# Optimization experiments

Hardware: AMD Instinct MI355X
Metric: run time of the kernel (lower is better)

Reference implementation:

```python
import jax, jax.numpy as jnp
import numpy as np

DIM = 1024
STATE = 64
HEADS = 8
EXPAND = 2
INNER = DIM * EXPAND          # 2048
HEAD_DIM = INNER // HEADS     # 256
KERNEL = 4
B, L = 2, 2048
EPS = 1e-5


def setup_inputs() -> dict:
    key = jax.random.key(0)
    ks = jax.random.split(key, 12)
    s = 0.02
    return {
        "input_tensor": jax.random.normal(ks[0], (B, L, DIM), jnp.float32),
        "Wx": jax.random.normal(ks[1], (INNER, DIM), jnp.float32) * s,
        "Wz": jax.random.normal(ks[2], (INNER, DIM), jnp.float32) * s,
        "conv_w": jax.random.normal(ks[3], (INNER, 1, KERNEL), jnp.float32) * s,
        "conv_b": jnp.zeros((INNER,), jnp.float32),
        "Wb": jax.random.normal(ks[4], (HEADS * STATE, INNER), jnp.float32) * s,
        "Wc": jax.random.normal(ks[5], (HEADS * STATE, INNER), jnp.float32) * s,
        "Wdt": jax.random.normal(ks[6], (HEADS, INNER), jnp.float32) * s,
        "b_dt": jnp.zeros((HEADS,), jnp.float32),
        "log_a": jnp.log(jnp.full((HEADS,), 0.5, jnp.float32)),
        "d_param": jnp.ones((HEADS,), jnp.float32),
        "gn_w": jnp.ones((INNER,), jnp.float32),
        "gn_b": jnp.zeros((INNER,), jnp.float32),
        "Wout": jax.random.normal(ks[7], (DIM, INNER), jnp.float32) * s,
    }


def _causal_conv(x, conv_w, conv_b):
    # x: (B, L, INNER); depthwise conv, kernel 4, left-pad 3 (causal)
    x_pad = jnp.pad(x, ((0, 0), (KERNEL - 1, 0), (0, 0)))
    w = conv_w[:, 0, :]  # (INNER, K)
    y = sum(x_pad[:, k:k + x.shape[1], :] * w[:, k] for k in range(KERNEL))
    return y + conv_b


def _ssd_scan(x, b, c, dt, a):
    # x: (B,L,H,P) b,c: (B,L,H,N) dt: (B,L,H) a: (H,)
    state0 = jnp.zeros((x.shape[0], HEADS, STATE, HEAD_DIM), x.dtype)

    def step(state, inp):
        x_t, b_t, c_t, dt_t = inp  # (B,H,P),(B,H,N),(B,H,N),(B,H)
        decay = jnp.exp(dt_t * a)[..., None, None]          # (B,H,1,1)
        b_bar = (dt_t[..., None] * b_t)                      # (B,H,N)
        state = decay * state + b_bar[..., None] * x_t[:, :, None, :]
        y_t = jnp.einsum("bhn,bhnp->bhp", c_t, state)
        return state, y_t

    xs = (x.transpose(1, 0, 2, 3), b.transpose(1, 0, 2, 3),
          c.transpose(1, 0, 2, 3), dt.transpose(1, 0, 2))
    _, ys = jax.lax.scan(step, state0, xs)  # ys: (L,B,H,P)
    return ys.transpose(1, 0, 2, 3)


def reference(input_tensor, Wx, Wz, conv_w, conv_b, Wb, Wc, Wdt, b_dt,
              log_a, d_param, gn_w, gn_b, Wout):
    bsz, seq, _ = input_tensor.shape
    x = input_tensor @ Wx.T               # (B,L,INNER)
    z = input_tensor @ Wz.T
    x = _causal_conv(x, conv_w, conv_b)
    x = jax.nn.silu(x)
    b = (x @ Wb.T).reshape(bsz, seq, HEADS, STATE)
    c = (x @ Wc.T).reshape(bsz, seq, HEADS, STATE)
    dt = jax.nn.softplus(x @ Wdt.T + b_dt)  # (B,L,H)
    xh = x.reshape(bsz, seq, HEADS, HEAD_DIM)
    a = -jnp.exp(log_a)
    y = _ssd_scan(xh, b, c, dt, a)
    y = y + d_param[None, None, :, None] * xh
    # GroupNorm(HEADS, INNER) applied on (B, C, L): normalize per (batch, group)
    # over (channels-in-group, sequence)
    yg = y  # (B, L, H, P) -- groups are contiguous channel blocks = heads
    mean = yg.mean(axis=(1, 3), keepdims=True)
    var = yg.var(axis=(1, 3), keepdims=True)
    yn = (yg - mean) / jnp.sqrt(var + EPS)
    yn = yn * gn_w.reshape(1, 1, HEADS, HEAD_DIM) + gn_b.reshape(1, 1, HEADS, HEAD_DIM)
    yn = yn.reshape(bsz, seq, INNER)
    out = yn * jax.nn.silu(z)
    return out @ Wout.T
```

## Files before the change

kernel.cpp:

```cpp
#include <hip/hip_runtime.h>
#include <math.h>

#define DIM_   1024
#define STATE_ 64
#define HEADS_ 8
#define INNER_ 2048
#define HDIM_  256
#define B_     2
#define L_     2048
#define M_     (B_*L_)
#define EPS_   1e-5f
#define Q_     64
#define NC_    (L_/Q_)
#define NCHUNK_ (B_*HEADS_*NC_)
#define BCS_   1024
#define XZS_   4096

typedef _Float16 f16;
typedef __attribute__((ext_vector_type(8))) _Float16 half8;
typedef __attribute__((ext_vector_type(4))) _Float16 half4;
typedef __attribute__((ext_vector_type(4))) float    f32x4;

__device__ __forceinline__ float siluf(float x) { return x / (1.f + expf(-x)); }

__device__ __forceinline__ void gload_lds16(const void* g, void* l) {
    __builtin_amdgcn_global_load_lds((const __attribute__((address_space(1))) void*)g,
                                     (__attribute__((address_space(3))) void*)l, 16, 0, 0);
}

__global__ __launch_bounds__(256) void cast_all(const float* __restrict__ in0,
                                                const float* __restrict__ Wx,
                                                const float* __restrict__ Wz,
                                                const float* __restrict__ Wb,
                                                const float* __restrict__ Wc,
                                                const float* __restrict__ Wout,
                                                f16* __restrict__ input_h,
                                                f16* __restrict__ wxz_h,
                                                f16* __restrict__ wbc_h,
                                                f16* __restrict__ wout_h) {
    int i = blockIdx.x * 256 + threadIdx.x;
    const float* src; f16* dst; int off;
    if      (i < 1048576) { src = in0;  dst = input_h;            off = i; }
    else if (i < 1572864) { src = Wx;   dst = wxz_h;              off = i - 1048576; }
    else if (i < 2097152) { src = Wz;   dst = wxz_h + 2097152;    off = i - 1572864; }
    else if (i < 2359296) { src = Wb;   dst = wbc_h;              off = i - 2097152; }
    else if (i < 2621440) { src = Wc;   dst = wbc_h + 1048576;    off = i - 2359296; }
    else                  { src = Wout; dst = wout_h;             off = i - 2621440; }
    float4 v = *(const float4*)&src[(size_t)off * 4];
    half4 o;
    o[0] = (f16)v.x; o[1] = (f16)v.y; o[2] = (f16)v.z; o[3] = (f16)v.w;
    *(half4*)&dst[(size_t)off * 4] = o;
}

template<int BN, bool OUTF16, bool SILUZ>
__global__ __launch_bounds__(256) void hgemm(const f16* __restrict__ A,
                                             const f16* __restrict__ W,
                                             void* __restrict__ Cout,
                                             int K, int N) {
    constexpr int N_FR = BN / 32;
    constexpr int NITER = (128 + BN) / 64;
    __shared__ f16 sA[128 * 32];
    __shared__ f16 sW[BN * 32];
    const int tid  = threadIdx.x;
    const int wid  = tid >> 6;
    const int lane = tid & 63;

    const int nwg = gridDim.x * gridDim.y;
    const int id0 = blockIdx.y * gridDim.x + blockIdx.x;
    const int cpx = nwg >> 3;
    const int id  = (id0 & 7) * cpx + (id0 >> 3);
    const int gxsh = __ffs(gridDim.x) - 1;
    const int bm = (id >> gxsh) * 128;
    const int bn = (id & (gridDim.x - 1)) * BN;

    const int wr = wid >> 1, wc = wid & 1;
    const int r  = lane & 15, kg = lane >> 4;

    const f16* gsrc[NITER];
    f16* ldst[NITER];
#pragma unroll
    for (int i = 0; i < NITER; ++i) {
        int slot = tid + i * 256;
        if (slot < 512) {
            int row = slot >> 2;
            int kgv = ((slot & 3) ^ ((row >> 1) & 3)) * 8;
            gsrc[i] = A + (size_t)(bm + row) * K + kgv;
        } else {
            int row = (slot - 512) >> 2;
            int kgv = ((slot & 3) ^ ((row >> 1) & 3)) * 8;
            gsrc[i] = W + (size_t)(bn + row) * K + kgv;
        }
        int slot0 = (tid & ~63) + i * 256;
        ldst[i] = (slot0 < 512) ? &sA[slot0 * 8] : &sW[(slot0 - 512) * 8];
    }

    int aoff[4], boff[N_FR];
#pragma unroll
    for (int m = 0; m < 4; ++m) {
        int arow = wr * 64 + m * 16 + r;
        aoff[m] = arow * 32 + ((kg ^ ((arow >> 1) & 3)) << 3);
    }
#pragma unroll
    for (int n = 0; n < N_FR; ++n) {
        int wrow = wc * (BN / 2) + n * 16 + r;
        boff[n] = wrow * 32 + ((kg ^ ((wrow >> 1) & 3)) << 3);
    }

    f32x4 acc[4][N_FR];
#pragma unroll
    for (int m = 0; m < 4; ++m)
#pragma unroll
        for (int n = 0; n < N_FR; ++n) acc[m][n] = (f32x4)0.f;

    for (int k0 = 0; k0 < K; k0 += 32) {
#pragma unroll
        for (int i = 0; i < NITER; ++i) gload_lds16(gsrc[i] + k0, ldst[i]);
        __syncthreads();
        half8 av[4], bv[N_FR];
#pragma unroll
        for (int m = 0; m < 4; ++m) av[m] = *(const half8*)&sA[aoff[m]];
#pragma unroll
        for (int n = 0; n < N_FR; ++n) bv[n] = *(const half8*)&sW[boff[n]];
#pragma unroll
        for (int m = 0; m < 4; ++m)
#pragma unroll
            for (int n = 0; n < N_FR; ++n)
                acc[m][n] = __builtin_amdgcn_mfma_f32_16x16x32_f16(av[m], bv[n], acc[m][n], 0, 0, 0);
        __syncthreads();
    }

#pragma unroll
    for (int m = 0; m < 4; ++m)
#pragma unroll
        for (int n = 0; n < N_FR; ++n) {
            int row0o = bm + wr * 64 + m * 16 + kg * 4;
            int col   = bn + wc * (BN / 2) + n * 16 + r;
#pragma unroll
            for (int j = 0; j < 4; ++j) {
                float v = acc[m][n][j];
                if (SILUZ && col >= INNER_) v = siluf(v);
                if (OUTF16) ((f16*)Cout)[(size_t)(row0o + j) * N + col] = (f16)v;
                else        ((float*)Cout)[(size_t)(row0o + j) * N + col] = v;
            }
        }
}

__global__ __launch_bounds__(256) void conv_silu_dt(const f16* __restrict__ xz,
                                                    const float* __restrict__ cw,
                                                    const float* __restrict__ cb,
                                                    const float* __restrict__ Wdt,
                                                    const float* __restrict__ bdt,
                                                    f16* __restrict__ xc,
                                                    float* __restrict__ dtb) {
    __shared__ float sred[4][HEADS_];
    const int m = blockIdx.x;
    const int tid = threadIdx.x;
    const int c8 = tid * 8;
    const int t = m & (L_ - 1);
    float acc[8];
    float4 wv[8];
#pragma unroll
    for (int j = 0; j < 8; ++j) { acc[j] = cb[c8 + j]; wv[j] = *(const float4*)&cw[(c8 + j) * 4]; }
#pragma unroll
    for (int k = 0; k < 4; ++k) {
        int tt = t - 3 + k;
        if (tt >= 0) {
            half8 xv = *(const half8*)&xz[(size_t)(m - 3 + k) * XZS_ + c8];
#pragma unroll
            for (int j = 0; j < 8; ++j) acc[j] += (float)xv[j] * ((const float*)&wv[j])[k];
        }
    }
    float xf[8];
    half8 o;
#pragma unroll
    for (int j = 0; j < 8; ++j) { xf[j] = siluf(acc[j]); o[j] = (f16)xf[j]; }
    *(half8*)&xc[(size_t)m * INNER_ + c8] = o;

    float p[HEADS_];
#pragma unroll
    for (int h = 0; h < HEADS_; ++h) {
        float4 w0 = *(const float4*)&Wdt[h * INNER_ + c8];
        float4 w1 = *(const float4*)&Wdt[h * INNER_ + c8 + 4];
        p[h] = xf[0]*w0.x + xf[1]*w0.y + xf[2]*w0.z + xf[3]*w0.w
             + xf[4]*w1.x + xf[5]*w1.y + xf[6]*w1.z + xf[7]*w1.w;
    }
#pragma unroll
    for (int h = 0; h < HEADS_; ++h)
#pragma unroll
        for (int off = 32; off > 0; off >>= 1)
            p[h] += __shfl_down(p[h], off, 64);
    if ((tid & 63) == 0) {
#pragma unroll
        for (int h = 0; h < HEADS_; ++h) sred[tid >> 6][h] = p[h];
    }
    __syncthreads();
    if (tid < 32) {
        float v = sred[tid >> 3][tid & 7];
        v += __shfl_down(v, 16, 32);
        v += __shfl_down(v, 8, 32);
        if (tid < 8) {
            float s = v + bdt[tid];
            dtb[(size_t)m * HEADS_ + tid] = (s > 20.f) ? s : log1pf(expf(s));
        }
    }
}

__global__ __launch_bounds__(256) void xpose_k(const f16* __restrict__ xc,
                                               f16* __restrict__ xT,
                                               float* __restrict__ gstat) {
    __shared__ f16 sT[64][72];
    const int blk = blockIdx.x;
    const int bh = blk >> 7;
    const int rem = blk & 127;
    const int tt = rem >> 2;
    const int pt = rem & 3;
    const int b = bh >> 3, h = bh & 7;
    const int tid = threadIdx.x;
    if (blk == 0 && tid < 2 * B_ * HEADS_) gstat[tid] = 0.f;
#pragma unroll
    for (int it = 0; it < 2; ++it) {
        int q = tid + it * 256;
        int tr = q >> 3;
        int p0 = (q & 7) * 8;
        half8 v = *(const half8*)&xc[(size_t)(b * L_ + tt * 64 + tr) * INNER_ + h * HDIM_ + pt * 64 + p0];
        *(half8*)&sT[tr][p0] = v;
    }
    __syncthreads();
#pragma unroll
    for (int it = 0; it < 2; ++it) {
        int q = tid + it * 256;
        int pr = q >> 3;
        int t0 = (q & 7) * 8;
        half8 v;
#pragma unroll
        for (int j = 0; j < 8; ++j) v[j] = sT[t0 + j][pr];
        *(half8*)&xT[((size_t)bh * HDIM_ + pt * 64 + pr) * L_ + tt * 64 + t0] = v;
    }
}

__global__ __launch_bounds__(256) void ssd12(const f16* __restrict__ bc,
                                             const float* __restrict__ dtb,
                                             const float* __restrict__ log_a,
                                             const f16* __restrict__ xT,
                                             f16* __restrict__ pbuf,
                                             f16* __restrict__ sloc,
                                             float* __restrict__ eAbuf,
                                             float* __restrict__ cdecay) {
    __shared__ float sA[Q_], sDt[Q_], sw[Q_];
    __shared__ f16 sB[Q_ * Q_];
    const int tid = threadIdx.x;
    const int chunk = blockIdx.x;
    const int bh = chunk / NC_;
    const int ck = chunk - bh * NC_;
    const int b = bh >> 3, h = bh & 7;
    const int m0 = b * L_ + ck * Q_;

    const int s0 = tid >> 3,        n00 = (tid & 7) * 8;
    const int s1 = (tid + 256) >> 3, n01 = (tid & 7) * 8;
    half8 bv0 = *(const half8*)&bc[(size_t)(m0 + s0) * BCS_ + h * STATE_ + n00];
    half8 bv1 = *(const half8*)&bc[(size_t)(m0 + s1) * BCS_ + h * STATE_ + n01];

    if (tid < 64) {
        float dt = dtb[(size_t)(m0 + tid) * HEADS_ + h];
        float a = -expf(log_a[h]);
        float x = dt * a;
#pragma unroll
        for (int off = 1; off < 64; off <<= 1) {
            float v = __shfl_up(x, off, 64);
            if (tid >= off) x += v;
        }
        float Alast = __shfl(x, 63, 64);
        sA[tid] = x;
        sDt[tid] = dt;
        sw[tid] = expf(Alast - x) * dt;
        eAbuf[(size_t)(m0 + tid) * HEADS_ + h] = expf(x);
        if (tid == 0) cdecay[chunk] = expf(Alast);
    }
    __syncthreads();

    {
        float w0 = sw[s0], w1 = sw[s1];
        half8 o0, o1;
#pragma unroll
        for (int j = 0; j < 8; ++j) { o0[j] = (f16)((float)bv0[j] * w0); o1[j] = (f16)((float)bv1[j] * w1); }
        *(half8*)&sB[s0 * Q_ + (n00 ^ ((s0 & 7) << 3))] = o0;
        *(half8*)&sB[s1 * Q_ + (n01 ^ ((s1 & 7) << 3))] = o1;
    }

    const int w = tid >> 6, lane = tid & 63;
    const int r = lane & 15, kg = lane >> 4;

    {
        const int ft = w;
        const f16* Crow = bc + (size_t)(m0 + ft * 16 + r) * BCS_ + 512 + h * STATE_;
        half8 a0 = *(const half8*)(Crow + kg * 8);
        half8 a1 = *(const half8*)(Crow + 32 + kg * 8);
#pragma unroll
        for (int fs = 0; fs < 4; ++fs) {
            const f16* Brow = bc + (size_t)(m0 + fs * 16 + r) * BCS_ + h * STATE_;
            half8 b0 = *(const half8*)(Brow + kg * 8);
            half8 b1 = *(const half8*)(Brow + 32 + kg * 8);
            f32x4 g = (f32x4)0.f;
            g = __builtin_amdgcn_mfma_f32_16x16x32_f16(a0, b0, g, 0, 0, 0);
            g = __builtin_amdgcn_mfma_f32_16x16x32_f16(a1, b1, g, 0, 0, 0);
            int s = fs * 16 + r;
            float As = sA[s], dts = sDt[s];
#pragma unroll
            for (int j = 0; j < 4; ++j) {
                int t = ft * 16 + kg * 4 + j;
                float val = (t >= s) ? g[j] * expf(sA[t] - As) * dts : 0.f;
                pbuf[((size_t)chunk * Q_ + t) * Q_ + s] = (f16)val;
            }
        }
    }
    __syncthreads();

    f32x4 acc[4][4];
#pragma unroll
    for (int i = 0; i < 4; ++i)
#pragma unroll
        for (int j = 0; j < 4; ++j) acc[i][j] = (f32x4)0.f;

#pragma unroll
    for (int kk = 0; kk < 2; ++kk) {
        half8 a[4], bfr[4];
#pragma unroll
        for (int pf = 0; pf < 4; ++pf) {
            int p = w * 64 + pf * 16 + r;
            a[pf] = *(const half8*)&xT[((size_t)bh * HDIM_ + p) * L_ + ck * Q_ + kk * 32 + kg * 8];
        }
#pragma unroll
        for (int nf = 0; nf < 4; ++nf) {
            int n = nf * 16 + r;
            half8 v;
#pragma unroll
            for (int j = 0; j < 8; ++j) {
                int s = kk * 32 + kg * 8 + j;
                v[j] = sB[s * Q_ + (n ^ (j << 3))];
            }
            bfr[nf] = v;
        }
#pragma unroll
        for (int pf = 0; pf < 4; ++pf)
#pragma unroll
            for (int nf = 0; nf < 4; ++nf)
                acc[pf][nf] = __builtin_amdgcn_mfma_f32_16x16x32_f16(a[pf], bfr[nf], acc[pf][nf], 0, 0, 0);
    }
#pragma unroll
    for (int pf = 0; pf < 4; ++pf)
#pragma unroll
        for (int nf = 0; nf < 4; ++nf) {
            int n = nf * 16 + r;
#pragma unroll
            for (int j = 0; j < 4; ++j) {
                int p = w * 64 + pf * 16 + kg * 4 + j;
                sloc[((size_t)chunk * HDIM_ + p) * STATE_ + n] = (f16)acc[pf][nf][j];
            }
        }
}

__global__ __launch_bounds__(256) void chunk_scan_k(f16* __restrict__ sloc,
                                                    const float* __restrict__ cdecay) {
    int bh = blockIdx.x >> 4;
    int el4 = (((blockIdx.x & 15) * 256 + threadIdx.x) << 2);
    float s0 = 0.f, s1 = 0.f, s2 = 0.f, s3 = 0.f;
    for (int c = 0; c < NC_; ++c) {
        size_t chunk = (size_t)bh * NC_ + c;
        f16* ptr = sloc + chunk * (size_t)(STATE_ * HDIM_) + el4;
        half4 v = *(const half4*)ptr;
        half4 o; o[0] = (f16)s0; o[1] = (f16)s1; o[2] = (f16)s2; o[3] = (f16)s3;
        *(half4*)ptr = o;
        float d = cdecay[chunk];
        s0 = d * s0 + (float)v[0];
        s1 = d * s1 + (float)v[1];
        s2 = d * s2 + (float)v[2];
        s3 = d * s3 + (float)v[3];
    }
}

__global__ __launch_bounds__(256) void ssd_phase3(const f16* __restrict__ bc,
                                                  const f16* __restrict__ pbuf,
                                                  const f16* __restrict__ xT,
                                                  const f16* __restrict__ sloc,
                                                  const f16* __restrict__ xch,
                                                  const float* __restrict__ eAbuf,
                                                  const float* __restrict__ dparam,
                                                  f16* __restrict__ ybuf,
                                                  float* __restrict__ gstats) {
    __shared__ float red[512];
    const int tid = threadIdx.x;
    const int chunk = blockIdx.x;
    const int bh = chunk / NC_;
    const int ck = chunk - bh * NC_;
    const int b = bh >> 3, h = bh & 7;
    const int m0 = b * L_ + ck * Q_;
    const int w = tid >> 6, lane = tid & 63;
    const int r = lane & 15, kg = lane >> 4;

    float eA[4];
#pragma unroll
    for (int ft = 0; ft < 4; ++ft)
        eA[ft] = eAbuf[(size_t)(m0 + ft * 16 + r) * HEADS_ + h];

    f32x4 acc[4][4];
#pragma unroll
    for (int i = 0; i < 4; ++i)
#pragma unroll
        for (int j = 0; j < 4; ++j) acc[i][j] = (f32x4)0.f;

#pragma unroll
    for (int ks = 0; ks < 4; ++ks) {
        half8 a[4], bfr[4];
#pragma unroll
        for (int ft = 0; ft < 4; ++ft) {
            int t = ft * 16 + r;
            if (ks < 2) {
                a[ft] = *(const half8*)&pbuf[((size_t)chunk * Q_ + t) * Q_ + ks * 32 + kg * 8];
            } else {
                half8 c = *(const half8*)&bc[(size_t)(m0 + t) * BCS_ + 512 + h * STATE_ + (ks - 2) * 32 + kg * 8];
                half8 sc;
#pragma unroll
                for (int j = 0; j < 8; ++j) sc[j] = (f16)(eA[ft] * (float)c[j]);
                a[ft] = sc;
            }
        }
#pragma unroll
        for (int pf = 0; pf < 4; ++pf) {
            int p = w * 64 + pf * 16 + r;
            if (ks < 2)
                bfr[pf] = *(const half8*)&xT[((size_t)bh * HDIM_ + p) * L_ + ck * Q_ + ks * 32 + kg * 8];
            else
                bfr[pf] = *(const half8*)&sloc[((size_t)chunk * HDIM_ + p) * STATE_ + (ks - 2) * 32 + kg * 8];
        }
#pragma unroll
        for (int ft = 0; ft < 4; ++ft)
#pragma unroll
            for (int pf = 0; pf < 4; ++pf)
                acc[ft][pf] = __builtin_amdgcn_mfma_f32_16x16x32_f16(a[ft], bfr[pf], acc[ft][pf], 0, 0, 0);
    }

    const float d = dparam[h];
    float lsum = 0.f, lsq = 0.f;
#pragma unroll
    for (int ft = 0; ft < 4; ++ft)
#pragma unroll
        for (int pf = 0; pf < 4; ++pf) {
            int p = w * 64 + pf * 16 + r;
#pragma unroll
            for (int j = 0; j < 4; ++j) {
                int t = ft * 16 + kg * 4 + j;
                size_t off = (size_t)(m0 + t) * INNER_ + h * HDIM_ + p;
                float y = acc[ft][pf][j] + d * (float)xch[off];
                ybuf[off] = (f16)y;
                lsum += y; lsq += y * y;
            }
        }
    __syncthreads();
    red[tid] = lsum; red[256 + tid] = lsq;
    __syncthreads();
    for (int st = 128; st > 0; st >>= 1) {
        if (tid < st) { red[tid] += red[tid + st]; red[256 + tid] += red[256 + tid + st]; }
        __syncthreads();
    }
    if (tid == 0) {
        atomicAdd(&gstats[bh * 2 + 0], red[0]);
        atomicAdd(&gstats[bh * 2 + 1], red[256]);
    }
}

__global__ __launch_bounds__(256) void gn_gate_h(const f16* __restrict__ ybuf,
                                                 const f16* __restrict__ xz,
                                                 const float* __restrict__ gstats,
                                                 const float* __restrict__ gnw,
                                                 const float* __restrict__ gnb,
                                                 f16* __restrict__ g) {
    int idx = blockIdx.x * 256 + threadIdx.x;
    int c8 = (idx & (INNER_/8 - 1)) * 8;
    int m = idx >> 8;
    int bh = (m >> 11) * HEADS_ + (c8 >> 8);
    const float cnt = (float)(L_ * HDIM_);
    float mean = gstats[bh*2] / cnt;
    float var  = gstats[bh*2+1] / cnt - mean*mean;
    float rstd = rsqrtf(var + EPS_);
    size_t off = (size_t)m * INNER_ + c8;
    half8 yv = *(const half8*)&ybuf[off];
    half8 zv = *(const half8*)&xz[(size_t)m * XZS_ + INNER_ + c8];
    float4 w0 = *(const float4*)&gnw[c8], w1 = *(const float4*)&gnw[c8+4];
    float4 b0 = *(const float4*)&gnb[c8], b1 = *(const float4*)&gnb[c8+4];
    float wv[8] = {w0.x, w0.y, w0.z, w0.w, w1.x, w1.y, w1.z, w1.w};
    float bv[8] = {b0.x, b0.y, b0.z, b0.w, b1.x, b1.y, b1.z, b1.w};
    half8 o;
#pragma unroll
    for (int j = 0; j < 8; ++j) {
        float v = ((float)yv[j] - mean) * rstd * wv[j] + bv[j];
        o[j] = (f16)(v * (float)zv[j]);
    }
    *(half8*)&g[off] = o;
}

extern "C" void kernel_launch(void* const* d_in, const int* in_sizes, int n_in,
                              void* d_out, int out_size, void* d_ws, size_t ws_size,
                              hipStream_t stream) {
    const float* input  = (const float*)d_in[0];
    const float* Wx     = (const float*)d_in[1];
    const float* Wz     = (const float*)d_in[2];
    const float* conv_w = (const float*)d_in[3];
    const float* conv_b = (const float*)d_in[4];
    const float* Wb     = (const float*)d_in[5];
    const float* Wc     = (const float*)d_in[6];
    const float* Wdt    = (const float*)d_in[7];
    const float* b_dt   = (const float*)d_in[8];
    const float* log_a  = (const float*)d_in[9];
    const float* d_par  = (const float*)d_in[10];
    const float* gn_w   = (const float*)d_in[11];
    const float* gn_b   = (const float*)d_in[12];
    const float* Wout   = (const float*)d_in[13];
    float* out = (float*)d_out;

    float* ws = (float*)d_ws;
    size_t off = 0;
    auto alloc = [&](size_t nfloats) { float* p = ws + off; off += (nfloats + 63) & ~(size_t)63; return p; };
    f16* input_h = (f16*)alloc((size_t)M_*DIM_/2);
    f16* wxz_h   = (f16*)alloc((size_t)XZS_*DIM_/2);
    f16* wbc_h   = (f16*)alloc((size_t)BCS_*INNER_/2);
    f16* wout_h  = (f16*)alloc((size_t)DIM_*INNER_/2);
    f16* xz_h    = (f16*)alloc((size_t)M_*XZS_/2);
    f16* xconv_h = (f16*)alloc((size_t)M_*INNER_/2);
    f16* xT_h    = (f16*)alloc((size_t)M_*INNER_/2);
    f16* gbuf_h  = (f16*)alloc((size_t)M_*INNER_/2);
    f16* bcmat_h = (f16*)alloc((size_t)M_*BCS_/2);
    f16* pbuf_h  = (f16*)alloc((size_t)NCHUNK_*Q_*Q_/2);
    f16* sloc_h  = (f16*)alloc((size_t)NCHUNK_*STATE_*HDIM_/2);
    f16* ybuf_h  = (f16*)alloc((size_t)M_*INNER_/2);
    float* dtb   = alloc((size_t)M_*HEADS_);
    float* eAb   = alloc((size_t)M_*HEADS_);
    float* cdec  = alloc((size_t)NCHUNK_);
    float* gstat = alloc((size_t)2*B_*HEADS_);

    dim3 blk(256);

    cast_all<<<12288, blk, 0, stream>>>(input, Wx, Wz, Wb, Wc, Wout,
                                        input_h, wxz_h, wbc_h, wout_h);
    hgemm<128,true,true><<<dim3(XZS_/128, M_/128), blk, 0, stream>>>(input_h, wxz_h, xz_h, DIM_, XZS_);
    conv_silu_dt<<<M_, blk, 0, stream>>>(xz_h, conv_w, conv_b, Wdt, b_dt, xconv_h, dtb);
    hgemm<64,true,false><<<dim3(BCS_/64, M_/128), blk, 0, stream>>>(xconv_h, wbc_h, bcmat_h, INNER_, BCS_);
    xpose_k<<<2048, blk, 0, stream>>>(xconv_h, xT_h, gstat);
    ssd12<<<NCHUNK_, blk, 0, stream>>>(bcmat_h, dtb, log_a, xT_h, pbuf_h, sloc_h, eAb, cdec);
    chunk_scan_k<<<256, blk, 0, stream>>>(sloc_h, cdec);
    ssd_phase3<<<NCHUNK_, blk, 0, stream>>>(bcmat_h, pbuf_h, xT_h, sloc_h, xconv_h,
                                            eAb, d_par, ybuf_h, gstat);
    gn_gate_h<<<(M_*(INNER_/8))/256, blk, 0, stream>>>(ybuf_h, xz_h, gstat, gn_w, gn_b, gbuf_h);
    hgemm<64,false,false><<<dim3(DIM_/64, M_/128), blk, 0, stream>>>(gbuf_h, wout_h, out, INNER_, DIM_);
}
```

Baseline: 363.2 us.

## Add 256x256 multi-stage GEMM for input projection and fold D skip into P

Replaces the first projection GEMM with a new 512-thread kernel that uses 256x256 tiles and a 4-slot LDS ring fed by direct global-to-LDS loads three stages ahead. It also drops the XCD-aware block swizzle from the generic GEMM. The D*x skip term moves into the diagonal of the intra-chunk P matrix, so phase 3 no longer re-reads the conv output. Risks include lower occupancy from 128 KB of LDS, and f16 rounding of the diagonal, now holding D plus the decay term.

```diff
diff --git a/kernel.cpp b/kernel.cpp
--- a/kernel.cpp
+++ b/kernel.cpp
@@ -52,7 +52,114 @@
     *(half4*)&dst[(size_t)off * 4] = o;
 }
 
-template<int BN, bool OUTF16, bool SILUZ>
+__global__ __launch_bounds__(512) void hgemm8p(const f16* __restrict__ A,
+                                               const f16* __restrict__ W,
+                                               f16* __restrict__ Cout,
+                                               int K, int N) {
+    __shared__ f16 lds[65536];
+    const int tid = threadIdx.x;
+    const int wid = tid >> 6, lane = tid & 63;
+    const int wm = wid >> 2, wn = wid & 3;
+    const int r = lane & 15, kg = lane >> 4;
+    const int bm = blockIdx.y * 256, bn = blockIdx.x * 256;
+
+    const int srow = tid >> 2;
+    const int scol = ((tid & 3) ^ ((srow >> 1) & 3)) * 8;
+    const f16* ga0 = A + (size_t)(bm + srow) * K + scol;
+    const f16* ga1 = A + (size_t)(bm + 128 + srow) * K + scol;
+    const f16* gw0 = W + (size_t)(bn + srow) * K + scol;
+    const f16* gw1 = W + (size_t)(bn + 128 + srow) * K + scol;
+    const int dbase = (tid & ~63) * 8;
+
+    int aoff[8], boff[4];
+#pragma unroll
+    for (int mf = 0; mf < 8; ++mf) {
+        int rr = wm * 128 + mf * 16 + r;
+        aoff[mf] = rr * 32 + ((kg ^ ((rr >> 1) & 3)) << 3);
+    }
+#pragma unroll
+    for (int nf = 0; nf < 4; ++nf) {
+        int wr = wn * 64 + nf * 16 + r;
+        boff[nf] = 8192 + wr * 32 + ((kg ^ ((wr >> 1) & 3)) << 3);
+    }
+
+    f32x4 acc[8][4];
+#pragma unroll
+    for (int mf = 0; mf < 8; ++mf)
+#pragma unroll
+        for (int nf = 0; nf < 4; ++nf) acc[mf][nf] = (f32x4)0.f;
+
+    const int KT = K >> 5;
+
+#pragma unroll
+    for (int kt = 0; kt < 3; ++kt) {
+        f16* base = &lds[(kt & 3) * 16384];
+        int ko = kt << 5;
+        gload_lds16(ga0 + ko, base + dbase);
+        gload_lds16(ga1 + ko, base + 4096 + dbase);
+        gload_lds16(gw0 + ko, base + 8192 + dbase);
+        gload_lds16(gw1 + ko, base + 12288 + dbase);
+    }
+    asm volatile("s_waitcnt vmcnt(8)" ::: "memory");
+    __builtin_amdgcn_s_barrier();
+    asm volatile("" ::: "memory");
+
+    for (int kt = 0; kt < KT; ++kt) {
+        f16* ring = &lds[(kt & 3) * 16384];
+        const bool st = (kt + 3) < KT;
+        f16* sbase = &lds[((kt + 3) & 3) * 16384];
+        const int sko = (kt + 3) << 5;
+
+        if (st) {
+            gload_lds16(ga0 + sko, sbase + dbase);
+            gload_lds16(ga1 + sko, sbase + 4096 + dbase);
+        }
+        half8 bfr[4], afr[4];
+#pragma unroll
+        for (int nf = 0; nf < 4; ++nf) bfr[nf] = *(const half8*)&ring[boff[nf]];
+#pragma unroll
+        for (int mf = 0; mf < 4; ++mf) afr[mf] = *(const half8*)&ring[aoff[mf]];
+#pragma unroll
+        for (int mf = 0; mf < 4; ++mf)
+#pragma unroll
+            for (int nf = 0; nf < 4; ++nf)
+                acc[mf][nf] = __builtin_amdgcn_mfma_f32_16x16x32_f16(afr[mf], bfr[nf], acc[mf][nf], 0, 0, 0);
+
+        if (st) {
+            gload_lds16(gw0 + sko, sbase + 8192 + dbase);
+            gload_lds16(gw1 + sko, sbase + 12288 + dbase);
+        }
+#pragma unroll
+        for (int mf = 0; mf < 4; ++mf) afr[mf] = *(const half8*)&ring[aoff[4 + mf]];
+#pragma unroll
+        for (int mf = 0; mf < 4; ++mf)
+#pragma unroll
+            for (int nf = 0; nf < 4; ++nf)
+                acc[4 + mf][nf] = __builtin_amdgcn_mfma_f32_16x16x32_f16(afr[mf], bfr[nf], acc[4 + mf][nf], 0, 0, 0);
+
+        if (kt + 1 < KT) {
+            asm volatile("s_waitcnt vmcnt(8)" ::: "memory");
+            __builtin_amdgcn_s_barrier();
+            asm volatile("" ::: "memory");
+        }
+    }
+
+#pragma unroll
+    for (int mf = 0; mf < 8; ++mf)
+#pragma unroll
+        for (int nf = 0; nf < 4; ++nf) {
+            int row = bm + wm * 128 + mf * 16 + kg * 4;
+            int col = bn + wn * 64 + nf * 16 + r;
+#pragma unroll
+            for (int j = 0; j < 4; ++j) {
+                float v = acc[mf][nf][j];
+                if (col >= INNER_) v = siluf(v);
+                Cout[(size_t)(row + j) * N + col] = (f16)v;
+            }
+        }
+}
+
+template<int BN, bool OUTF16>
 __global__ __launch_bounds__(256) void hgemm(const f16* __restrict__ A,
                                              const f16* __restrict__ W,
                                              void* __restrict__ Cout,
@@ -64,15 +171,8 @@
     const int tid  = threadIdx.x;
     const int wid  = tid >> 6;
     const int lane = tid & 63;
-
-    const int nwg = gridDim.x * gridDim.y;
-    const int id0 = blockIdx.y * gridDim.x + blockIdx.x;
-    const int cpx = nwg >> 3;
-    const int id  = (id0 & 7) * cpx + (id0 >> 3);
-    const int gxsh = __ffs(gridDim.x) - 1;
-    const int bm = (id >> gxsh) * 128;
-    const int bn = (id & (gridDim.x - 1)) * BN;
-
+    const int bm = blockIdx.y * 128;
+    const int bn = blockIdx.x * BN;
     const int wr = wid >> 1, wc = wid & 1;
     const int r  = lane & 15, kg = lane >> 4;
 
@@ -138,7 +238,6 @@
 #pragma unroll
             for (int j = 0; j < 4; ++j) {
                 float v = acc[m][n][j];
-                if (SILUZ && col >= INNER_) v = siluf(v);
                 if (OUTF16) ((f16*)Cout)[(size_t)(row0o + j) * N + col] = (f16)v;
                 else        ((float*)Cout)[(size_t)(row0o + j) * N + col] = v;
             }
@@ -241,6 +340,7 @@
 __global__ __launch_bounds__(256) void ssd12(const f16* __restrict__ bc,
                                              const float* __restrict__ dtb,
                                              const float* __restrict__ log_a,
+                                             const float* __restrict__ dparam,
                                              const f16* __restrict__ xT,
                                              f16* __restrict__ pbuf,
                                              f16* __restrict__ sloc,
@@ -291,6 +391,7 @@
     const int r = lane & 15, kg = lane >> 4;
 
     {
+        const float dpar = dparam[h];
         const int ft = w;
         const f16* Crow = bc + (size_t)(m0 + ft * 16 + r) * BCS_ + 512 + h * STATE_;
         half8 a0 = *(const half8*)(Crow + kg * 8);
@@ -309,6 +410,7 @@
             for (int j = 0; j < 4; ++j) {
                 int t = ft * 16 + kg * 4 + j;
                 float val = (t >= s) ? g[j] * expf(sA[t] - As) * dts : 0.f;
+                if (t == s) val += dpar;
                 pbuf[((size_t)chunk * Q_ + t) * Q_ + s] = (f16)val;
             }
         }
@@ -382,11 +484,10 @@
                                                   const f16* __restrict__ pbuf,
                                                   const f16* __restrict__ xT,
                                                   const f16* __restrict__ sloc,
-                                                  const f16* __restrict__ xch,
                                                   const float* __restrict__ eAbuf,
-                                                  const float* __restrict__ dparam,
-                                                  f16* __restrict__ ybuf,
+                                                  float* __restrict__ ybuf16_,
                                                   float* __restrict__ gstats) {
+    f16* ybuf = (f16*)ybuf16_;
     __shared__ float red[512];
     const int tid = threadIdx.x;
     const int chunk = blockIdx.x;
@@ -439,7 +540,6 @@
                 acc[ft][pf] = __builtin_amdgcn_mfma_f32_16x16x32_f16(a[ft], bfr[pf], acc[ft][pf], 0, 0, 0);
     }
 
-    const float d = dparam[h];
     float lsum = 0.f, lsq = 0.f;
 #pragma unroll
     for (int ft = 0; ft < 4; ++ft)
@@ -450,7 +550,7 @@
             for (int j = 0; j < 4; ++j) {
                 int t = ft * 16 + kg * 4 + j;
                 size_t off = (size_t)(m0 + t) * INNER_ + h * HDIM_ + p;
-                float y = acc[ft][pf][j] + d * (float)xch[off];
+                float y = acc[ft][pf][j];
                 ybuf[off] = (f16)y;
                 lsum += y; lsq += y * y;
             }
@@ -541,14 +641,14 @@
 
     cast_all<<<12288, blk, 0, stream>>>(input, Wx, Wz, Wb, Wc, Wout,
                                         input_h, wxz_h, wbc_h, wout_h);
-    hgemm<128,true,true><<<dim3(XZS_/128, M_/128), blk, 0, stream>>>(input_h, wxz_h, xz_h, DIM_, XZS_);
+    hgemm8p<<<dim3(XZS_/256, M_/256), dim3(512), 0, stream>>>(input_h, wxz_h, xz_h, DIM_, XZS_);
     conv_silu_dt<<<M_, blk, 0, stream>>>(xz_h, conv_w, conv_b, Wdt, b_dt, xconv_h, dtb);
-    hgemm<64,true,false><<<dim3(BCS_/64, M_/128), blk, 0, stream>>>(xconv_h, wbc_h, bcmat_h, INNER_, BCS_);
+    hgemm<64,true><<<dim3(BCS_/64, M_/128), blk, 0, stream>>>(xconv_h, wbc_h, bcmat_h, INNER_, BCS_);
     xpose_k<<<2048, blk, 0, stream>>>(xconv_h, xT_h, gstat);
-    ssd12<<<NCHUNK_, blk, 0, stream>>>(bcmat_h, dtb, log_a, xT_h, pbuf_h, sloc_h, eAb, cdec);
+    ssd12<<<NCHUNK_, blk, 0, stream>>>(bcmat_h, dtb, log_a, d_par, xT_h, pbuf_h, sloc_h, eAb, cdec);
     chunk_scan_k<<<256, blk, 0, stream>>>(sloc_h, cdec);
-    ssd_phase3<<<NCHUNK_, blk, 0, stream>>>(bcmat_h, pbuf_h, xT_h, sloc_h, xconv_h,
-                                            eAb, d_par, ybuf_h, gstat);
+    ssd_phase3<<<NCHUNK_, blk, 0, stream>>>(bcmat_h, pbuf_h, xT_h, sloc_h,
+                                            eAb, (float*)ybuf_h, gstat);
     gn_gate_h<<<(M_*(INNER_/8))/256, blk, 0, stream>>>(ybuf_h, xz_h, gstat, gn_w, gn_b, gbuf_h);
-    hgemm<64,false,false><<<dim3(DIM_/64, M_/128), blk, 0, stream>>>(gbuf_h, wout_h, out, INNER_, DIM_);
-}
+    hgemm<64,false><<<dim3(DIM_/64, M_/128), blk, 0, stream>>>(gbuf_h, wout_h, out, INNER_, DIM_);
+}
```

Result: faster. 345.7 us (-4.8%).
